# Kernel tuning notes

Hardware: AMD Instinct MI355X
Metric: run time of the kernel (lower is better)

The kernel has to match this reference:

```python
import jax, jax.numpy as jnp
import numpy as np

B, L, F, H, D, Z, NF = 256, 256, 38, 512, 512, 16, 20
LOG2PI = float(np.log(2.0 * np.pi))


def setup_inputs() -> dict:
    ks = jax.random.split(jax.random.key(0), 32)
    def p(i, shape, s=0.05):
        return jax.random.normal(ks[i], shape, jnp.float32) * s
    return {
        "x": jax.random.normal(ks[0], (B, L, F), jnp.float32),
        "phi_Wih": p(1, (3 * H, F)), "phi_Whh": p(2, (3 * H, H)),
        "phi_bih": p(3, (3 * H,)), "phi_bhh": p(4, (3 * H,)),
        "phi_W1": p(5, (D, H + Z)), "phi_b1": p(6, (D,)),
        "phi_W2": p(7, (D, D)), "phi_b2": p(8, (D,)),
        "zloc_W": p(9, (Z, D)), "zloc_b": p(10, (Z,)),
        "zscale_W": p(11, (Z, D)), "zscale_b": p(12, (Z,)),
        "pu": p(13, (NF, Z)), "pw": p(14, (NF, Z)), "pb": p(15, (NF,)),
        "th_Wih": p(16, (3 * H, Z)), "th_Whh": p(17, (3 * H, H)),
        "th_bih": p(18, (3 * H,)), "th_bhh": p(19, (3 * H,)),
        "th_W1": p(20, (D, H)), "th_b1": p(21, (D,)),
        "th_W2": p(22, (D, D)), "th_b2": p(23, (D,)),
        "xloc_W": p(24, (F, D)), "xloc_b": p(25, (F,)),
        "xscale_W": p(26, (F, D)), "xscale_b": p(27, (F,)),
    }


def _gru(x, h, Wih, Whh, bih, bhh):
    # torch.nn.GRUCell, gate order (r, z, n)
    gi = x @ Wih.T + bih
    gh = h @ Whh.T + bhh
    ir, iz, inn = jnp.split(gi, 3, axis=-1)
    hr, hz, hn = jnp.split(gh, 3, axis=-1)
    r = jax.nn.sigmoid(ir + hr)
    z = jax.nn.sigmoid(iz + hz)
    n = jnp.tanh(inn + r * hn)
    return (1.0 - z) * n + z * h


def _normal_lp(x, loc, scale):
    return -0.5 * ((x - loc) / scale) ** 2 - jnp.log(scale) - 0.5 * LOG2PI


def _forward(x, phi_Wih, phi_Whh, phi_bih, phi_bhh, phi_W1, phi_b1, phi_W2, phi_b2,
             zloc_W, zloc_b, zscale_W, zscale_b, pu, pw, pb,
             th_Wih, th_Whh, th_bih, th_bhh, th_W1, th_b1, th_W2, th_b2,
             xloc_W, xloc_b, xscale_W, xscale_b):
    b, l, f = x.shape
    z_dim = zloc_b.shape[0]
    h_dim = phi_bih.shape[0] // 3
    # fixed rsample noise (reference determinism): z posterior base sample + prior sample
    kz, kp = jax.random.split(jax.random.key(42))
    eps_z = jax.random.normal(kz, (l, b, z_dim), x.dtype)
    eps_p = jax.random.normal(kp, (l, b, z_dim), x.dtype)
    xs = jnp.swapaxes(x, 0, 1)  # [L, B, F]

    # Pyro Planar: u_hat = u + (softplus(w.u) - 1 - w.u) * w / ||w||^2
    wnorm2 = jnp.sum(pw * pw, axis=-1)                     # [NF]
    wu = jnp.sum(pw * pu, axis=-1)                         # [NF]
    uhat = pu + ((jax.nn.softplus(wu) - 1.0 - wu) / wnorm2)[:, None] * pw  # [NF, Z]
    uhat_w = jnp.sum(uhat * pw, axis=-1)                   # [NF]

    def flows(z0):
        def fstep(z, fp):
            w, uh, bb, uw = fp
            a = jnp.tanh(z @ w + bb)                       # [B]
            z_new = z + uh[None, :] * a[:, None]
            ld = jnp.log(jnp.abs(1.0 + (1.0 - a * a) * uw) + 1e-12)  # [B]
            return z_new, ld
        z_fin, lds = jax.lax.scan(fstep, z0, (pw, uhat, pb, uhat_w))
        return z_fin, jnp.sum(lds)

    def step(carry, inp):
        phi_h, th_h, zt, recon, kld = carry
        xt, ez, ep = inp
        phi_h = _gru(xt, phi_h, phi_Wih, phi_Whh, phi_bih, phi_bhh)
        h1 = jax.nn.relu(jnp.concatenate([phi_h, zt], axis=-1) @ phi_W1.T + phi_b1)
        h2 = h1 @ phi_W2.T + phi_b2
        z_loc = h2 @ zloc_W.T + zloc_b
        z_scale = jax.nn.softplus(h2 @ zscale_W.T + zscale_b) + 1e-6
        z0 = z_loc + z_scale * ez
        base_lp = jnp.sum(-0.5 * ez * ez - jnp.log(z_scale) - 0.5 * LOG2PI)
        zt_new, logdet = flows(z0)
        th_h = _gru(zt_new, th_h, th_Wih, th_Whh, th_bih, th_bhh)
        g1 = jax.nn.relu(th_h @ th_W1.T + th_b1)
        g2 = g1 @ th_W2.T + th_b2
        y_loc = g2 @ xloc_W.T + xloc_b
        y_scale = jax.nn.softplus(g2 @ xscale_W.T + xscale_b) + 1e-6
        recon = recon - jnp.sum(_normal_lp(xt, y_loc, y_scale))
        # prior log_prob of its own rsample depends only on eps (loc cancels)
        prior_lp = jnp.sum(-0.5 * ep * ep - 0.5 * LOG2PI)
        kld = kld + (base_lp - logdet) - prior_lp
        return (phi_h, th_h, zt_new, recon, kld), y_loc

    init = (jnp.zeros((b, h_dim), x.dtype), jnp.zeros((b, h_dim), x.dtype),
            jnp.zeros((b, z_dim), x.dtype), jnp.zeros((), x.dtype), jnp.zeros((), x.dtype))
    (_, _, _, recon, kld), y_loc = jax.lax.scan(step, init, (xs, eps_z, eps_p))
    return jnp.swapaxes(y_loc, 0, 1), recon, kld


def reference(x, phi_Wih, phi_Whh, phi_bih, phi_bhh, phi_W1, phi_b1, phi_W2, phi_b2,
              zloc_W, zloc_b, zscale_W, zscale_b, pu, pw, pb,
              th_Wih, th_Whh, th_bih, th_bhh, th_W1, th_b1, th_W2, th_b2,
              xloc_W, xloc_b, xscale_W, xscale_b):
    return _forward(x, phi_Wih, phi_Whh, phi_bih, phi_bhh, phi_W1, phi_b1, phi_W2, phi_b2,
                    zloc_W, zloc_b, zscale_W, zscale_b, pu, pw, pb,
                    th_Wih, th_Whh, th_bih, th_bhh, th_W1, th_b1, th_W2, th_b2,
                    xloc_W, xloc_b, xscale_W, xscale_b)
```

## Files before the change

### kernel.cpp

```cpp
#include <hip/hip_runtime.h>
#include <stdint.h>
#include <math.h>

namespace {

constexpr int B = 256, L = 256, F = 38, H = 512, D = 512, Z = 16, NF = 20;
constexpr float LOG2PI_F = 1.8378770664093453f;
constexpr int LBZ = L * B * Z;
constexpr int HALF = LBZ / 2;
constexpr int HB = H * B;
constexpr int DB = D * B;
constexpr int ZB = Z * B;
constexpr int LFB = L * F * B;
constexpr int TC = 32;


__device__ __forceinline__ float sigmoidf_(float x) {
  return 1.0f / (1.0f + expf(-x));
}
__device__ __forceinline__ float softplusf_(float x) {
  return fmaxf(x, 0.0f) + log1pf(expf(-fabsf(x)));
}

__device__ __forceinline__ void waveReduceAtomicAdd(float* dst, float v, int tid) {
  #pragma unroll
  for (int off = 32; off > 0; off >>= 1) v += __shfl_down(v, off, 64);
  if ((tid & 63) == 0) atomicAdd(dst, v);
}


__host__ __device__ inline uint32_t rotl32_(uint32_t x, int d) {
  return (x << d) | (x >> (32 - d));
}

__host__ __device__ inline void threefry2x32_(uint32_t k0, uint32_t k1,
                                              uint32_t x0, uint32_t x1,
                                              uint32_t& o0, uint32_t& o1) {
  const uint32_t ks2 = k0 ^ k1 ^ 0x1BD11BDAu;
  uint32_t v0 = x0 + k0;
  uint32_t v1 = x1 + k1;
#define TF_RND(r) { v0 += v1; v1 = rotl32_(v1, r); v1 ^= v0; }
  TF_RND(13) TF_RND(15) TF_RND(26) TF_RND(6)
  v0 += k1;  v1 += ks2 + 1u;
  TF_RND(17) TF_RND(29) TF_RND(16) TF_RND(24)
  v0 += ks2; v1 += k0 + 2u;
  TF_RND(13) TF_RND(15) TF_RND(26) TF_RND(6)
  v0 += k0;  v1 += k1 + 3u;
  TF_RND(17) TF_RND(29) TF_RND(16) TF_RND(24)
  v0 += k1;  v1 += ks2 + 4u;
  TF_RND(13) TF_RND(15) TF_RND(26) TF_RND(6)
  v0 += ks2; v1 += k0 + 5u;
#undef TF_RND
  o0 = v0; o1 = v1;
}

__device__ __forceinline__ float erfinv_f_(float x) {
  float w = -log1pf(-x * x);
  float p;
  if (w < 5.0f) {
    w -= 2.5f;
    p = 2.81022636e-08f;
    p = fmaf(p, w, 3.43273939e-07f);
    p = fmaf(p, w, -3.5233877e-06f);
    p = fmaf(p, w, -4.39150654e-06f);
    p = fmaf(p, w, 0.00021858087f);
    p = fmaf(p, w, -0.00125372503f);
    p = fmaf(p, w, -0.00417768164f);
    p = fmaf(p, w, 0.246640727f);
    p = fmaf(p, w, 1.50140941f);
  } else {
    w = sqrtf(w) - 3.0f;
    p = -0.000200214257f;
    p = fmaf(p, w, 0.000100950558f);
    p = fmaf(p, w, 0.00134934322f);
    p = fmaf(p, w, -0.00367342844f);
    p = fmaf(p, w, 0.00573950773f);
    p = fmaf(p, w, -0.0076224613f);
    p = fmaf(p, w, 0.00943887047f);
    p = fmaf(p, w, 1.00167406f);
    p = fmaf(p, w, 2.83297682f);
  }
  return p * x;
}

__device__ __forceinline__ float bits_to_normal_(uint32_t bits) {
  uint32_t m = (bits >> 9) | 0x3f800000u;
  float f = __uint_as_float(m) - 1.0f;
  float u = f * 2.0f + (-0.99999994f);
  u = fmaxf(-0.99999994f, u);
  return 1.41421356f * erfinv_f_(u);
}

__device__ __forceinline__ float flows_dev(float zv[Z], const float* __restrict__ pu,
                                           const float* __restrict__ pw,
                                           const float* __restrict__ pb) {
  float ld = 0.0f;
  for (int f = 0; f < NF; ++f) {
    const float* w = pw + f * Z;
    const float* u = pu + f * Z;
    float wn2 = 0.0f, wu = 0.0f;
    #pragma unroll
    for (int i = 0; i < Z; ++i) { wn2 = fmaf(w[i], w[i], wn2); wu = fmaf(w[i], u[i], wu); }
    float coef = (softplusf_(wu) - 1.0f - wu) / wn2;
    float a_in = pb[f];
    #pragma unroll
    for (int i = 0; i < Z; ++i) a_in = fmaf(zv[i], w[i], a_in);
    float a = tanhf(a_in);
    float uw = 0.0f;
    #pragma unroll
    for (int i = 0; i < Z; ++i) {
      float uh = fmaf(coef, w[i], u[i]);
      uw = fmaf(uh, w[i], uw);
      zv[i] = fmaf(uh, a, zv[i]);
    }
    ld += logf(fabsf(1.0f + (1.0f - a * a) * uw) + 1e-12f);
  }
  return ld;
}


__global__ __launch_bounds__(256) void k_transpose_x(const float* __restrict__ x,
                                                     float* __restrict__ xT) {
  int idx = blockIdx.x * blockDim.x + threadIdx.x;
  int f = idx % F;
  int t = (idx / F) % L;
  int b = idx / (F * L);
  xT[(t * F + f) * B + b] = x[idx];
}

__global__ __launch_bounds__(256) void k_noise(float* __restrict__ eps_z,
                                               float* __restrict__ kld_acc,
                                               uint32_t kz0, uint32_t kz1,
                                               uint32_t kp0, uint32_t kp1) {
  int i = blockIdx.x * blockDim.x + threadIdx.x;
  uint32_t a0, a1, b0, b1;
  threefry2x32_(kz0, kz1, (uint32_t)i, (uint32_t)(i + HALF), a0, a1);
  float ez0 = bits_to_normal_(a0);
  float ez1 = bits_to_normal_(a1);
  eps_z[i] = ez0;
  eps_z[i + HALF] = ez1;
  threefry2x32_(kp0, kp1, (uint32_t)i, (uint32_t)(i + HALF), b0, b1);
  float ep0 = bits_to_normal_(b0);
  float ep1 = bits_to_normal_(b1);
  float local = -0.5f * (ez0 * ez0 + ez1 * ez1) + 0.5f * (ep0 * ep0 + ep1 * ep1);
  waveReduceAtomicAdd(kld_acc, local, threadIdx.x);
}

__global__ void k_finalize(const float* __restrict__ acc, float* __restrict__ out) {
  out[(size_t)B * L * F] = acc[1];
  out[(size_t)B * L * F + 1] = acc[0];
}

__global__ __launch_bounds__(256) void k_compose(
    const float* __restrict__ A, const float* __restrict__ bA,
    const float* __restrict__ W2, const float* __restrict__ b2,
    float* __restrict__ Wc, float* __restrict__ bc) {
  const int r = blockIdx.x;
  const int k = threadIdx.x;
  float acc0 = 0.f, acc1 = 0.f;
  for (int j = 0; j < D; ++j) {
    float a = A[(size_t)r * D + j];
    acc0 = fmaf(a, W2[(size_t)j * D + k], acc0);
    acc1 = fmaf(a, W2[(size_t)j * D + k + 256], acc1);
  }
  Wc[(size_t)r * D + k] = acc0;
  Wc[(size_t)r * D + k + 256] = acc1;
  float accb = 0.f;
  for (int j = k; j < D; j += 256) accb += A[(size_t)r * D + j] * b2[j];
  __shared__ float s[256];
  s[k] = accb;
  __syncthreads();
  for (int off = 128; off > 0; off >>= 1) {
    if (k < off) s[k] += s[k + off];
    __syncthreads();
  }
  if (k == 0) bc[r] = s[0] + bA[r];
}


struct GruArgs {
  const float* xin;
  const float* hT;
  const float* Wih;
  const float* Whh;
  const float* bih;
  const float* bhh;
  float* hout;
  float* zT_out;
  const float* pu;
  const float* pw;
  const float* pb;
  float* kld_acc;
  int w0h;
};

template<bool THETA>
__device__ __forceinline__ void gru_dev(const GruArgs& A,
                                        float (&red)[4][4][8][64]) {
  const int tid = threadIdx.x;
  const int lane = tid & 63;
  const int wv = __builtin_amdgcn_readfirstlane(tid >> 6);
  const int j0 = blockIdx.x * 8;
  const int b0 = blockIdx.y * 64;
  const int b = b0 + lane;
  constexpr int K1 = THETA ? Z : F;

  float accR[8], accZ[8], accNX[8], accNH[8];
  #pragma unroll
  for (int r = 0; r < 8; ++r) { accR[r] = 0.f; accZ[r] = 0.f; accNX[r] = 0.f; accNH[r] = 0.f; }

  float zv[Z];
  float ld = 0.0f;

  if (wv == 0) {
    const float* wr = A.Wih + (size_t)(0 * H + j0) * K1;
    const float* wz = A.Wih + (size_t)(1 * H + j0) * K1;
    const float* wn = A.Wih + (size_t)(2 * H + j0) * K1;
    if (THETA) {
      #pragma unroll
      for (int i = 0; i < Z; ++i) zv[i] = A.xin[i * B + b];
      ld = flows_dev(zv, A.pu, A.pw, A.pb);
      #pragma unroll
      for (int k = 0; k < Z; k += 4) {
        #pragma unroll
        for (int r = 0; r < 8; ++r) {
          const float4 w0 = *(const float4*)(wr + r * K1 + k);
          const float4 w1 = *(const float4*)(wz + r * K1 + k);
          const float4 w2 = *(const float4*)(wn + r * K1 + k);
          accR[r]  = fmaf(w0.x, zv[k], fmaf(w0.y, zv[k+1], fmaf(w0.z, zv[k+2], fmaf(w0.w, zv[k+3], accR[r]))));
          accZ[r]  = fmaf(w1.x, zv[k], fmaf(w1.y, zv[k+1], fmaf(w1.z, zv[k+2], fmaf(w1.w, zv[k+3], accZ[r]))));
          accNX[r] = fmaf(w2.x, zv[k], fmaf(w2.y, zv[k+1], fmaf(w2.z, zv[k+2], fmaf(w2.w, zv[k+3], accNX[r]))));
        }
      }
    } else {
      for (int k = 0; k < K1; ++k) {
        float a = A.xin[k * B + b];
        #pragma unroll
        for (int r = 0; r < 8; ++r) {
          accR[r]  = fmaf(wr[r * K1 + k], a, accR[r]);
          accZ[r]  = fmaf(wz[r * K1 + k], a, accZ[r]);
          accNX[r] = fmaf(wn[r * K1 + k], a, accNX[r]);
        }
      }
    }
  }

  const int rest = (H - A.w0h) / 3;
  const int hlo = (wv == 0) ? 0 : A.w0h + (wv - 1) * rest;
  const int hhi = (wv == 0) ? A.w0h : hlo + rest;
  {
    const float* vr = A.Whh + (size_t)(0 * H + j0) * H;
    const float* vz = A.Whh + (size_t)(1 * H + j0) * H;
    const float* vn = A.Whh + (size_t)(2 * H + j0) * H;
    #pragma unroll 2
    for (int k = hlo; k < hhi; k += 4) {
      const float a0 = A.hT[(size_t)(k + 0) * B + b];
      const float a1 = A.hT[(size_t)(k + 1) * B + b];
      const float a2 = A.hT[(size_t)(k + 2) * B + b];
      const float a3 = A.hT[(size_t)(k + 3) * B + b];
      #pragma unroll
      for (int r = 0; r < 8; ++r) {
        const float4 w0 = *(const float4*)(vr + (size_t)r * H + k);
        const float4 w1 = *(const float4*)(vz + (size_t)r * H + k);
        const float4 w2 = *(const float4*)(vn + (size_t)r * H + k);
        accR[r]  = fmaf(w0.x, a0, fmaf(w0.y, a1, fmaf(w0.z, a2, fmaf(w0.w, a3, accR[r]))));
        accZ[r]  = fmaf(w1.x, a0, fmaf(w1.y, a1, fmaf(w1.z, a2, fmaf(w1.w, a3, accZ[r]))));
        accNH[r] = fmaf(w2.x, a0, fmaf(w2.y, a1, fmaf(w2.z, a2, fmaf(w2.w, a3, accNH[r]))));
      }
    }
  }

  #pragma unroll
  for (int r = 0; r < 8; ++r) {
    red[wv][0][r][lane] = accR[r];
    red[wv][1][r][lane] = accZ[r];
    red[wv][2][r][lane] = accNX[r];
    red[wv][3][r][lane] = accNH[r];
  }

  if (THETA) {
    if (wv == 0 && blockIdx.x == 0) {
      #pragma unroll
      for (int i = 0; i < Z; ++i) A.zT_out[i * B + b] = zv[i];
      waveReduceAtomicAdd(A.kld_acc, -ld, lane);
    }
  }

  __syncthreads();

  #pragma unroll
  for (int it = tid; it < 512; it += 256) {
    const int r = it >> 6, l = it & 63;
    float sR = 0.f, sZ = 0.f, sNX = 0.f, sNH = 0.f;
    #pragma unroll
    for (int w = 0; w < 4; ++w) {
      sR  += red[w][0][r][l];
      sZ  += red[w][1][r][l];
      sNX += red[w][2][r][l];
      sNH += red[w][3][r][l];
    }
    const int j = j0 + r;
    const int bb = b0 + l;
    const float rg = sigmoidf_(sR + A.bih[j] + A.bhh[j]);
    const float zg = sigmoidf_(sZ + A.bih[H + j] + A.bhh[H + j]);
    const float ng = tanhf(sNX + A.bih[2 * H + j] + rg * (sNH + A.bhh[2 * H + j]));
    const float hp = A.hT[(size_t)j * B + bb];
    A.hout[(size_t)j * B + bb] = (1.0f - zg) * ng + zg * hp;
  }
}

__global__ __launch_bounds__(256) void k_gru_dual(GruArgs phi, GruArgs th, int mode) {
  __shared__ float red[4][4][8][64];
  const bool isTheta = (mode == 1) || (mode == 2 && blockIdx.z == 1);
  if (isTheta) gru_dev<true>(th, red);
  else         gru_dev<false>(phi, red);
}

__global__ __launch_bounds__(256) void k_lin(
    const float* __restrict__ A1, int K1v, long sA1,
    const float* __restrict__ A2, int K2v,
    const float* __restrict__ W, const float* __restrict__ bias,
    float* __restrict__ outp, long sOut, int relu) {
  const int tid = threadIdx.x;
  const int lane = tid & 63;
  const int wv = __builtin_amdgcn_readfirstlane(tid >> 6);
  const int r0 = blockIdx.x * 8;
  const int b0 = blockIdx.y * 64;
  const int b = b0 + lane;
  const int Kv = K1v + K2v;
  const float* A1p = A1 + (size_t)blockIdx.z * sA1;
  float* outpp = outp + (size_t)blockIdx.z * sOut;
  const int klo = wv * (Kv >> 2);
  const int khi = klo + (Kv >> 2);

  float acc[8];
  #pragma unroll
  for (int r = 0; r < 8; ++r) acc[r] = 0.f;

  const float* wbase = W + (size_t)r0 * Kv;
  {
    const int hi = khi < K1v ? khi : K1v;
    #pragma unroll 4
    for (int k = klo; k < hi; k += 4) {
      const float a0 = A1p[(size_t)(k + 0) * B + b];
      const float a1 = A1p[(size_t)(k + 1) * B + b];
      const float a2 = A1p[(size_t)(k + 2) * B + b];
      const float a3 = A1p[(size_t)(k + 3) * B + b];
      #pragma unroll
      for (int r = 0; r < 8; ++r) {
        const float4 w4 = *(const float4*)(wbase + (size_t)r * Kv + k);
        acc[r] = fmaf(w4.x, a0, fmaf(w4.y, a1, fmaf(w4.z, a2, fmaf(w4.w, a3, acc[r]))));
      }
    }
  }
  if (K2v) {
    const int lo = klo > K1v ? klo : K1v;
    for (int k = lo; k < khi; k += 4) {
      const float a0 = A2[(size_t)(k - K1v + 0) * B + b];
      const float a1 = A2[(size_t)(k - K1v + 1) * B + b];
      const float a2 = A2[(size_t)(k - K1v + 2) * B + b];
      const float a3 = A2[(size_t)(k - K1v + 3) * B + b];
      #pragma unroll
      for (int r = 0; r < 8; ++r) {
        const float4 w4 = *(const float4*)(wbase + (size_t)r * Kv + k);
        acc[r] = fmaf(w4.x, a0, fmaf(w4.y, a1, fmaf(w4.z, a2, fmaf(w4.w, a3, acc[r]))));
      }
    }
  }

  __shared__ float red[4][8][64];
  #pragma unroll
  for (int r = 0; r < 8; ++r) red[wv][r][lane] = acc[r];
  __syncthreads();

  #pragma unroll
  for (int it = tid; it < 512; it += 256) {
    int r = it >> 6, l = it & 63;
    float s = red[0][r][l] + red[1][r][l] + red[2][r][l] + red[3][r][l] + bias[r0 + r];
    if (relu) s = fmaxf(s, 0.f);
    outpp[(size_t)(r0 + r) * B + b0 + l] = s;
  }
}

__global__ __launch_bounds__(256) void k_zhead(
    const float* __restrict__ h1T,
    const float* __restrict__ Wzl, const float* __restrict__ bzl,
    const float* __restrict__ Wzs, const float* __restrict__ bzs,
    const float* __restrict__ eps_t,
    float* __restrict__ z0T, float* __restrict__ kld_acc) {
  const int tid = threadIdx.x;
  const int lane = tid & 63;
  const int wv = __builtin_amdgcn_readfirstlane(tid >> 6);
  const int z0q = blockIdx.x * 4;
  const int b0 = blockIdx.y * 64;
  const int b = b0 + lane;
  const int klo = wv * (D >> 2), khi = klo + (D >> 2);

  const float* wp[8];
  #pragma unroll
  for (int i = 0; i < 8; ++i) {
    int zz = z0q + (i >> 1);
    wp[i] = ((i & 1) ? Wzs : Wzl) + (size_t)zz * D;
  }
  float acc[8];
  #pragma unroll
  for (int i = 0; i < 8; ++i) acc[i] = 0.f;
  #pragma unroll 4
  for (int k = klo; k < khi; k += 4) {
    const float a0 = h1T[(size_t)(k + 0) * B + b];
    const float a1 = h1T[(size_t)(k + 1) * B + b];
    const float a2 = h1T[(size_t)(k + 2) * B + b];
    const float a3 = h1T[(size_t)(k + 3) * B + b];
    #pragma unroll
    for (int i = 0; i < 8; ++i) {
      const float4 w4 = *(const float4*)(wp[i] + k);
      acc[i] = fmaf(w4.x, a0, fmaf(w4.y, a1, fmaf(w4.z, a2, fmaf(w4.w, a3, acc[i]))));
    }
  }

  __shared__ float red[4][8][64];
  #pragma unroll
  for (int i = 0; i < 8; ++i) red[wv][i][lane] = acc[i];
  __syncthreads();

  int zi = tid >> 6, l = tid & 63;
  int zz = z0q + zi;
  int bb = b0 + l;
  float sl = red[0][2 * zi][l] + red[1][2 * zi][l] + red[2][2 * zi][l] + red[3][2 * zi][l]
             + bzl[zz];
  float ss = red[0][2 * zi + 1][l] + red[1][2 * zi + 1][l] + red[2][2 * zi + 1][l]
             + red[3][2 * zi + 1][l] + bzs[zz];
  float scale = softplusf_(ss) + 1e-6f;
  float ez = eps_t[bb * Z + zz];
  z0T[zz * B + bb] = sl + scale * ez;
  waveReduceAtomicAdd(kld_acc, -logf(scale), tid);
}

__global__ __launch_bounds__(256) void k_yhead(
    const float* __restrict__ g1base, long sG1, int t_base,
    const float* __restrict__ Wyl, const float* __restrict__ byl,
    const float* __restrict__ Wys, const float* __restrict__ bys,
    const float* __restrict__ xT,
    float* __restrict__ out_yloc, float* __restrict__ recon_acc) {
  const int tid = threadIdx.x;
  const int lane = tid & 63;
  const int wv = __builtin_amdgcn_readfirstlane(tid >> 6);
  const int t = t_base + blockIdx.z;
  const float* g1T = g1base + (size_t)blockIdx.z * sG1;
  const int f0 = blockIdx.x * 4;
  const int b0 = blockIdx.y * 64;
  const int b = b0 + lane;
  const int klo = wv * (D >> 2), khi = klo + (D >> 2);

  const float* wp[8];
  #pragma unroll
  for (int i = 0; i < 8; ++i) {
    int ff = f0 + (i >> 1);
    int fc = ff < F ? ff : 0;
    wp[i] = ((i & 1) ? Wys : Wyl) + (size_t)fc * D;
  }
  float acc[8];
  #pragma unroll
  for (int i = 0; i < 8; ++i) acc[i] = 0.f;
  #pragma unroll 4
  for (int k = klo; k < khi; k += 4) {
    const float a0 = g1T[(size_t)(k + 0) * B + b];
    const float a1 = g1T[(size_t)(k + 1) * B + b];
    const float a2 = g1T[(size_t)(k + 2) * B + b];
    const float a3 = g1T[(size_t)(k + 3) * B + b];
    #pragma unroll
    for (int i = 0; i < 8; ++i) {
      const float4 w4 = *(const float4*)(wp[i] + k);
      acc[i] = fmaf(w4.x, a0, fmaf(w4.y, a1, fmaf(w4.z, a2, fmaf(w4.w, a3, acc[i]))));
    }
  }

  __shared__ float red[4][8][64];
  #pragma unroll
  for (int i = 0; i < 8; ++i) red[wv][i][lane] = acc[i];
  __syncthreads();

  int fi = tid >> 6, l = tid & 63;
  int ff = f0 + fi;
  int bb = b0 + l;
  float nl = 0.0f;
  if (ff < F) {
    float loc = red[0][2 * fi][l] + red[1][2 * fi][l] + red[2][2 * fi][l] + red[3][2 * fi][l]
                + byl[ff];
    float sp = red[0][2 * fi + 1][l] + red[1][2 * fi + 1][l] + red[2][2 * fi + 1][l]
               + red[3][2 * fi + 1][l] + bys[ff];
    float scale = softplusf_(sp) + 1e-6f;
    out_yloc[((size_t)bb * L + t) * F + ff] = loc;
    float xv = xT[((size_t)t * F + ff) * B + bb];
    float d = (xv - loc) / scale;
    nl = 0.5f * d * d + logf(scale) + 0.5f * LOG2PI_F;
  }
  waveReduceAtomicAdd(recon_acc, nl, tid);
}

}

extern "C" void kernel_launch(void* const* d_in, const int* in_sizes, int n_in,
                              void* d_out, int out_size, void* d_ws, size_t ws_size,
                              hipStream_t stream) {
  const float* x        = (const float*)d_in[0];
  const float* phi_Wih  = (const float*)d_in[1];
  const float* phi_Whh  = (const float*)d_in[2];
  const float* phi_bih  = (const float*)d_in[3];
  const float* phi_bhh  = (const float*)d_in[4];
  const float* phi_W1   = (const float*)d_in[5];
  const float* phi_b1   = (const float*)d_in[6];
  const float* phi_W2   = (const float*)d_in[7];
  const float* phi_b2   = (const float*)d_in[8];
  const float* zloc_W   = (const float*)d_in[9];
  const float* zloc_b   = (const float*)d_in[10];
  const float* zscale_W = (const float*)d_in[11];
  const float* zscale_b = (const float*)d_in[12];
  const float* pu       = (const float*)d_in[13];
  const float* pw       = (const float*)d_in[14];
  const float* pb       = (const float*)d_in[15];
  const float* th_Wih   = (const float*)d_in[16];
  const float* th_Whh   = (const float*)d_in[17];
  const float* th_bih   = (const float*)d_in[18];
  const float* th_bhh   = (const float*)d_in[19];
  const float* th_W1    = (const float*)d_in[20];
  const float* th_b1    = (const float*)d_in[21];
  const float* th_W2    = (const float*)d_in[22];
  const float* th_b2    = (const float*)d_in[23];
  const float* xloc_W   = (const float*)d_in[24];
  const float* xloc_b   = (const float*)d_in[25];
  const float* xscale_W = (const float*)d_in[26];
  const float* xscale_b = (const float*)d_in[27];

  float* out = (float*)d_out;
  float* ws = (float*)d_ws;

  float* acc   = ws;
  float* eps_z = ws + 64;
  float* xT    = eps_z + LBZ;
  float* hphi0 = xT + LFB;
  float* hphi1 = hphi0 + HB;
  float* zT    = hphi1 + HB;
  float* z0T   = zT + ZB;
  float* h1T   = z0T + ZB;
  float* g1T   = h1T + DB;
  float* Wzl   = g1T + DB;
  float* Wzs   = Wzl + Z * D;
  float* bzl   = Wzs + Z * D;
  float* bzs   = bzl + 64;
  float* Wyl   = bzs + 64;
  float* Wys   = Wyl + F * D;
  float* byl   = Wys + F * D;
  float* bys   = byl + 64;
  float* tailbase = bys + 64;

  size_t floatsA = (size_t)(tailbase - ws) + (size_t)(L + 1) * HB + (size_t)TC * DB;
  bool pathA = ws_size >= floatsA * sizeof(float);

  float* th_all = tailbase;
  float* g1_c   = th_all + (size_t)(L + 1) * HB;
  float* hth0   = tailbase;
  float* hth1   = tailbase + HB;

  hipMemsetAsync(acc, 0, 2 * sizeof(float), stream);
  hipMemsetAsync(hphi0, 0, (size_t)HB * sizeof(float), stream);
  hipMemsetAsync(zT, 0, (size_t)ZB * sizeof(float), stream);
  if (pathA) hipMemsetAsync(th_all, 0, (size_t)HB * sizeof(float), stream);
  else       hipMemsetAsync(hth1, 0, (size_t)HB * sizeof(float), stream);

  uint32_t a0, a1, b0, b1;
  threefry2x32_(0u, 42u, 0u, 2u, a0, a1);
  threefry2x32_(0u, 42u, 1u, 3u, b0, b1);
  const uint32_t kz0 = a0, kz1 = b0, kp0 = a1, kp1 = b1;

  k_transpose_x<<<(B * L * F) / 256, 256, 0, stream>>>(x, xT);
  k_noise<<<HALF / 256, 256, 0, stream>>>(eps_z, acc, kz0, kz1, kp0, kp1);

  k_compose<<<Z, 256, 0, stream>>>(zloc_W, zloc_b, phi_W2, phi_b2, Wzl, bzl);
  k_compose<<<Z, 256, 0, stream>>>(zscale_W, zscale_b, phi_W2, phi_b2, Wzs, bzs);
  k_compose<<<F, 256, 0, stream>>>(xloc_W, xloc_b, th_W2, th_b2, Wyl, byl);
  k_compose<<<F, 256, 0, stream>>>(xscale_W, xscale_b, th_W2, th_b2, Wys, bys);

  const dim3 gLin(D / 8, B / 64, 1);
  const dim3 gZ(Z / 4, B / 64, 1);

  for (int t = 0; t <= L; ++t) {
    const bool hasPhi = (t < L);
    const bool hasTh  = (t >= 1);

    GruArgs pa = {};
    GruArgs ta = {};
    float* phi_new = (t & 1) ? hphi0 : hphi1;
    if (hasPhi) {
      pa.xin  = xT + (size_t)t * F * B;
      pa.hT   = (t & 1) ? hphi1 : hphi0;
      pa.hout = phi_new;
      pa.Wih = phi_Wih; pa.Whh = phi_Whh; pa.bih = phi_bih; pa.bhh = phi_bhh;
      pa.w0h = 92;
    }
    float* th_new = nullptr;
    if (hasTh) {
      ta.xin  = z0T;
      ta.hT   = pathA ? th_all + (size_t)(t - 1) * HB
                      : ((t & 1) ? hth1 : hth0);
      th_new  = pathA ? th_all + (size_t)t * HB
                      : ((t & 1) ? hth0 : hth1);
      ta.hout = th_new;
      ta.Wih = th_Wih; ta.Whh = th_Whh; ta.bih = th_bih; ta.bhh = th_bhh;
      ta.zT_out = zT; ta.pu = pu; ta.pw = pw; ta.pb = pb; ta.kld_acc = acc;
      ta.w0h = 80;
    }

    const int mode = (hasPhi && hasTh) ? 2 : (hasTh ? 1 : 0);
    dim3 gG(H / 8, B / 64, mode == 2 ? 2 : 1);
    k_gru_dual<<<gG, 256, 0, stream>>>(pa, ta, mode);

    if (hasPhi) {
      k_lin<<<gLin, 256, 0, stream>>>(phi_new, H, 0, zT, Z, phi_W1, phi_b1, h1T, 0, 1);
      k_zhead<<<gZ, 256, 0, stream>>>(h1T, Wzl, bzl, Wzs, bzs,
                                      eps_z + (size_t)t * B * Z, z0T, acc);
    }

    if (!pathA && hasTh) {
      k_lin<<<gLin, 256, 0, stream>>>(th_new, H, 0, nullptr, 0, th_W1, th_b1, g1T, 0, 1);
      dim3 gy((F + 3) / 4, B / 64, 1);
      k_yhead<<<gy, 256, 0, stream>>>(g1T, 0, t - 1, Wyl, byl, Wys, bys,
                                      xT, out, acc + 1);
    }
  }

  if (pathA) {
    for (int c = 0; c < L / TC; ++c) {
      const float* thh = th_all + (size_t)(c * TC + 1) * HB;
      dim3 g1(D / 8, B / 64, TC);
      k_lin<<<g1, 256, 0, stream>>>(thh, H, HB, nullptr, 0, th_W1, th_b1, g1_c, DB, 1);
      dim3 gy((F + 3) / 4, B / 64, TC);
      k_yhead<<<gy, 256, 0, stream>>>(g1_c, DB, c * TC, Wyl, byl, Wys, bys,
                                      xT, out, acc + 1);
    }
  }

  k_finalize<<<1, 1, 0, stream>>>(acc, out);
}
```

Measured before the change: 23.90 ms.

## Replace per-timestep kernel launches with a persistent kernel using grid barriers

```diff
diff --git a/kernel.cpp b/kernel.cpp
--- a/kernel.cpp
+++ b/kernel.cpp
@@ -12,7 +12,7 @@
 constexpr int DB = D * B;
 constexpr int ZB = Z * B;
 constexpr int LFB = L * F * B;
-constexpr int TC = 32;
+constexpr int GRIDN = 512;
 
 
 __device__ __forceinline__ float sigmoidf_(float x) {
@@ -26,6 +26,25 @@
   #pragma unroll
   for (int off = 32; off > 0; off >>= 1) v += __shfl_down(v, off, 64);
   if ((tid & 63) == 0) atomicAdd(dst, v);
+}
+
+__device__ __forceinline__ void grid_sync_(uint32_t* bar) {
+  __syncthreads();
+  if (threadIdx.x == 0) {
+    __threadfence();
+    uint32_t g = __hip_atomic_load(&bar[1], __ATOMIC_RELAXED, __HIP_MEMORY_SCOPE_AGENT);
+    uint32_t a = __hip_atomic_fetch_add(&bar[0], 1u, __ATOMIC_RELAXED, __HIP_MEMORY_SCOPE_AGENT);
+    if (a == (uint32_t)(GRIDN - 1)) {
+      __hip_atomic_store(&bar[0], 0u, __ATOMIC_RELAXED, __HIP_MEMORY_SCOPE_AGENT);
+      __threadfence();
+      __hip_atomic_fetch_add(&bar[1], 1u, __ATOMIC_RELAXED, __HIP_MEMORY_SCOPE_AGENT);
+    } else {
+      while (__hip_atomic_load(&bar[1], __ATOMIC_RELAXED, __HIP_MEMORY_SCOPE_AGENT) == g)
+        __builtin_amdgcn_s_sleep(2);
+    }
+    __threadfence();
+  }
+  __syncthreads();
 }
 
 
@@ -177,31 +196,19 @@
   if (k == 0) bc[r] = s[0] + bA[r];
 }
 
-
-struct GruArgs {
-  const float* xin;
-  const float* hT;
-  const float* Wih;
-  const float* Whh;
-  const float* bih;
-  const float* bhh;
-  float* hout;
-  float* zT_out;
-  const float* pu;
-  const float* pw;
-  const float* pb;
-  float* kld_acc;
-  int w0h;
-};
-
 template<bool THETA>
-__device__ __forceinline__ void gru_dev(const GruArgs& A,
-                                        float (&red)[4][4][8][64]) {
+__device__ __forceinline__ void gru_phase(
+    int blk2, const float* __restrict__ xin, const float* __restrict__ hT,
+    const float* __restrict__ Wih, const float* __restrict__ Whh,
+    const float* __restrict__ bih, const float* __restrict__ bhh,
+    float* __restrict__ hout, float* zT_out,
+    const float* pu, const float* pw, const float* pb, float* kld_acc,
+    int w0h, float (&red)[4][4][8][64]) {
   const int tid = threadIdx.x;
   const int lane = tid & 63;
   const int wv = __builtin_amdgcn_readfirstlane(tid >> 6);
-  const int j0 = blockIdx.x * 8;
-  const int b0 = blockIdx.y * 64;
+  const int j0 = (blk2 >> 2) * 8;
+  const int b0 = (blk2 & 3) * 64;
   const int b = b0 + lane;
   constexpr int K1 = THETA ? Z : F;
 
@@ -213,13 +220,13 @@
   float ld = 0.0f;
 
   if (wv == 0) {
-    const float* wr = A.Wih + (size_t)(0 * H + j0) * K1;
-    const float* wz = A.Wih + (size_t)(1 * H + j0) * K1;
-    const float* wn = A.Wih + (size_t)(2 * H + j0) * K1;
+    const float* wr = Wih + (size_t)(0 * H + j0) * K1;
+    const float* wz = Wih + (size_t)(1 * H + j0) * K1;
+    const float* wn = Wih + (size_t)(2 * H + j0) * K1;
     if (THETA) {
       #pragma unroll
-      for (int i = 0; i < Z; ++i) zv[i] = A.xin[i * B + b];
-      ld = flows_dev(zv, A.pu, A.pw, A.pb);
+      for (int i = 0; i < Z; ++i) zv[i] = xin[i * B + b];
+      ld = flows_dev(zv, pu, pw, pb);
       #pragma unroll
       for (int k = 0; k < Z; k += 4) {
         #pragma unroll
@@ -234,7 +241,7 @@
       }
     } else {
       for (int k = 0; k < K1; ++k) {
-        float a = A.xin[k * B + b];
+        float a = xin[k * B + b];
         #pragma unroll
         for (int r = 0; r < 8; ++r) {
           accR[r]  = fmaf(wr[r * K1 + k], a, accR[r]);
@@ -245,19 +252,19 @@
     }
   }
 
-  const int rest = (H - A.w0h) / 3;
-  const int hlo = (wv == 0) ? 0 : A.w0h + (wv - 1) * rest;
-  const int hhi = (wv == 0) ? A.w0h : hlo + rest;
+  const int rest = (H - w0h) / 3;
+  const int hlo = (wv == 0) ? 0 : w0h + (wv - 1) * rest;
+  const int hhi = (wv == 0) ? w0h : hlo + rest;
   {
-    const float* vr = A.Whh + (size_t)(0 * H + j0) * H;
-    const float* vz = A.Whh + (size_t)(1 * H + j0) * H;
-    const float* vn = A.Whh + (size_t)(2 * H + j0) * H;
+    const float* vr = Whh + (size_t)(0 * H + j0) * H;
+    const float* vz = Whh + (size_t)(1 * H + j0) * H;
+    const float* vn = Whh + (size_t)(2 * H + j0) * H;
     #pragma unroll 2
     for (int k = hlo; k < hhi; k += 4) {
-      const float a0 = A.hT[(size_t)(k + 0) * B + b];
-      const float a1 = A.hT[(size_t)(k + 1) * B + b];
-      const float a2 = A.hT[(size_t)(k + 2) * B + b];
-      const float a3 = A.hT[(size_t)(k + 3) * B + b];
+      const float a0 = hT[(size_t)(k + 0) * B + b];
+      const float a1 = hT[(size_t)(k + 1) * B + b];
+      const float a2 = hT[(size_t)(k + 2) * B + b];
+      const float a3 = hT[(size_t)(k + 3) * B + b];
       #pragma unroll
       for (int r = 0; r < 8; ++r) {
         const float4 w0 = *(const float4*)(vr + (size_t)r * H + k);
@@ -279,10 +286,10 @@
   }
 
   if (THETA) {
-    if (wv == 0 && blockIdx.x == 0) {
+    if (wv == 0 && j0 == 0) {
       #pragma unroll
-      for (int i = 0; i < Z; ++i) A.zT_out[i * B + b] = zv[i];
-      waveReduceAtomicAdd(A.kld_acc, -ld, lane);
+      for (int i = 0; i < Z; ++i) zT_out[i * B + b] = zv[i];
+      waveReduceAtomicAdd(kld_acc, -ld, lane);
     }
   }
 
@@ -301,35 +308,26 @@
     }
     const int j = j0 + r;
     const int bb = b0 + l;
-    const float rg = sigmoidf_(sR + A.bih[j] + A.bhh[j]);
-    const float zg = sigmoidf_(sZ + A.bih[H + j] + A.bhh[H + j]);
-    const float ng = tanhf(sNX + A.bih[2 * H + j] + rg * (sNH + A.bhh[2 * H + j]));
-    const float hp = A.hT[(size_t)j * B + bb];
-    A.hout[(size_t)j * B + bb] = (1.0f - zg) * ng + zg * hp;
-  }
-}
-
-__global__ __launch_bounds__(256) void k_gru_dual(GruArgs phi, GruArgs th, int mode) {
-  __shared__ float red[4][4][8][64];
-  const bool isTheta = (mode == 1) || (mode == 2 && blockIdx.z == 1);
-  if (isTheta) gru_dev<true>(th, red);
-  else         gru_dev<false>(phi, red);
-}
-
-__global__ __launch_bounds__(256) void k_lin(
-    const float* __restrict__ A1, int K1v, long sA1,
+    const float rg = sigmoidf_(sR + bih[j] + bhh[j]);
+    const float zg = sigmoidf_(sZ + bih[H + j] + bhh[H + j]);
+    const float ng = tanhf(sNX + bih[2 * H + j] + rg * (sNH + bhh[2 * H + j]));
+    const float hp = hT[(size_t)j * B + bb];
+    hout[(size_t)j * B + bb] = (1.0f - zg) * ng + zg * hp;
+  }
+}
+
+__device__ __forceinline__ void lin8_phase(
+    int blk2, const float* __restrict__ A1, int K1v,
     const float* __restrict__ A2, int K2v,
     const float* __restrict__ W, const float* __restrict__ bias,
-    float* __restrict__ outp, long sOut, int relu) {
+    float* __restrict__ outp, int relu, float* shbase) {
   const int tid = threadIdx.x;
   const int lane = tid & 63;
   const int wv = __builtin_amdgcn_readfirstlane(tid >> 6);
-  const int r0 = blockIdx.x * 8;
-  const int b0 = blockIdx.y * 64;
+  const int r0 = (blk2 >> 2) * 8;
+  const int b0 = (blk2 & 3) * 64;
   const int b = b0 + lane;
   const int Kv = K1v + K2v;
-  const float* A1p = A1 + (size_t)blockIdx.z * sA1;
-  float* outpp = outp + (size_t)blockIdx.z * sOut;
   const int klo = wv * (Kv >> 2);
   const int khi = klo + (Kv >> 2);
 
@@ -342,10 +340,10 @@
     const int hi = khi < K1v ? khi : K1v;
     #pragma unroll 4
     for (int k = klo; k < hi; k += 4) {
-      const float a0 = A1p[(size_t)(k + 0) * B + b];
-      const float a1 = A1p[(size_t)(k + 1) * B + b];
-      const float a2 = A1p[(size_t)(k + 2) * B + b];
-      const float a3 = A1p[(size_t)(k + 3) * B + b];
+      const float a0 = A1[(size_t)(k + 0) * B + b];
+      const float a1 = A1[(size_t)(k + 1) * B + b];
+      const float a2 = A1[(size_t)(k + 2) * B + b];
+      const float a3 = A1[(size_t)(k + 3) * B + b];
       #pragma unroll
       for (int r = 0; r < 8; ++r) {
         const float4 w4 = *(const float4*)(wbase + (size_t)r * Kv + k);
@@ -368,31 +366,32 @@
     }
   }
 
-  __shared__ float red[4][8][64];
-  #pragma unroll
-  for (int r = 0; r < 8; ++r) red[wv][r][lane] = acc[r];
+  float* red = shbase;
+  #pragma unroll
+  for (int r = 0; r < 8; ++r) red[(wv * 8 + r) * 64 + lane] = acc[r];
   __syncthreads();
 
   #pragma unroll
   for (int it = tid; it < 512; it += 256) {
     int r = it >> 6, l = it & 63;
-    float s = red[0][r][l] + red[1][r][l] + red[2][r][l] + red[3][r][l] + bias[r0 + r];
+    float s = red[(0 * 8 + r) * 64 + l] + red[(1 * 8 + r) * 64 + l]
+            + red[(2 * 8 + r) * 64 + l] + red[(3 * 8 + r) * 64 + l] + bias[r0 + r];
     if (relu) s = fmaxf(s, 0.f);
-    outpp[(size_t)(r0 + r) * B + b0 + l] = s;
-  }
-}
-
-__global__ __launch_bounds__(256) void k_zhead(
-    const float* __restrict__ h1T,
+    outp[(size_t)(r0 + r) * B + b0 + l] = s;
+  }
+}
+
+__device__ __forceinline__ void zhead_phase(
+    int blk2, const float* __restrict__ h1T,
     const float* __restrict__ Wzl, const float* __restrict__ bzl,
     const float* __restrict__ Wzs, const float* __restrict__ bzs,
-    const float* __restrict__ eps_t,
-    float* __restrict__ z0T, float* __restrict__ kld_acc) {
+    const float* __restrict__ eps_t, float* __restrict__ z0T,
+    float* kld_acc, float* shbase) {
   const int tid = threadIdx.x;
   const int lane = tid & 63;
   const int wv = __builtin_amdgcn_readfirstlane(tid >> 6);
-  const int z0q = blockIdx.x * 4;
-  const int b0 = blockIdx.y * 64;
+  const int z0q = (blk2 >> 2) * 4;
+  const int b0 = (blk2 & 3) * 64;
   const int b = b0 + lane;
   const int klo = wv * (D >> 2), khi = klo + (D >> 2);
 
@@ -418,37 +417,35 @@
     }
   }
 
-  __shared__ float red[4][8][64];
-  #pragma unroll
-  for (int i = 0; i < 8; ++i) red[wv][i][lane] = acc[i];
+  float* red = shbase;
+  #pragma unroll
+  for (int i = 0; i < 8; ++i) red[(wv * 8 + i) * 64 + lane] = acc[i];
   __syncthreads();
 
   int zi = tid >> 6, l = tid & 63;
   int zz = z0q + zi;
   int bb = b0 + l;
-  float sl = red[0][2 * zi][l] + red[1][2 * zi][l] + red[2][2 * zi][l] + red[3][2 * zi][l]
-             + bzl[zz];
-  float ss = red[0][2 * zi + 1][l] + red[1][2 * zi + 1][l] + red[2][2 * zi + 1][l]
-             + red[3][2 * zi + 1][l] + bzs[zz];
+  float sl = red[(0 * 8 + 2 * zi) * 64 + l] + red[(1 * 8 + 2 * zi) * 64 + l]
+           + red[(2 * 8 + 2 * zi) * 64 + l] + red[(3 * 8 + 2 * zi) * 64 + l] + bzl[zz];
+  float ss = red[(0 * 8 + 2 * zi + 1) * 64 + l] + red[(1 * 8 + 2 * zi + 1) * 64 + l]
+           + red[(2 * 8 + 2 * zi + 1) * 64 + l] + red[(3 * 8 + 2 * zi + 1) * 64 + l] + bzs[zz];
   float scale = softplusf_(ss) + 1e-6f;
   float ez = eps_t[bb * Z + zz];
   z0T[zz * B + bb] = sl + scale * ez;
   waveReduceAtomicAdd(kld_acc, -logf(scale), tid);
 }
 
-__global__ __launch_bounds__(256) void k_yhead(
-    const float* __restrict__ g1base, long sG1, int t_base,
+__device__ __forceinline__ void yhead_phase(
+    int blk2, int t, const float* __restrict__ g1T,
     const float* __restrict__ Wyl, const float* __restrict__ byl,
     const float* __restrict__ Wys, const float* __restrict__ bys,
-    const float* __restrict__ xT,
-    float* __restrict__ out_yloc, float* __restrict__ recon_acc) {
+    const float* __restrict__ xT, float* __restrict__ out_yloc,
+    float* recon_acc, float* shbase) {
   const int tid = threadIdx.x;
   const int lane = tid & 63;
   const int wv = __builtin_amdgcn_readfirstlane(tid >> 6);
-  const int t = t_base + blockIdx.z;
-  const float* g1T = g1base + (size_t)blockIdx.z * sG1;
-  const int f0 = blockIdx.x * 4;
-  const int b0 = blockIdx.y * 64;
+  const int f0 = (blk2 >> 2) * 4;
+  const int b0 = (blk2 & 3) * 64;
   const int b = b0 + lane;
   const int klo = wv * (D >> 2), khi = klo + (D >> 2);
 
@@ -475,9 +472,9 @@
     }
   }
 
-  __shared__ float red[4][8][64];
-  #pragma unroll
-  for (int i = 0; i < 8; ++i) red[wv][i][lane] = acc[i];
+  float* red = shbase;
+  #pragma unroll
+  for (int i = 0; i < 8; ++i) red[(wv * 8 + i) * 64 + lane] = acc[i];
   __syncthreads();
 
   int fi = tid >> 6, l = tid & 63;
@@ -485,10 +482,10 @@
   int bb = b0 + l;
   float nl = 0.0f;
   if (ff < F) {
-    float loc = red[0][2 * fi][l] + red[1][2 * fi][l] + red[2][2 * fi][l] + red[3][2 * fi][l]
-                + byl[ff];
-    float sp = red[0][2 * fi + 1][l] + red[1][2 * fi + 1][l] + red[2][2 * fi + 1][l]
-               + red[3][2 * fi + 1][l] + bys[ff];
+    float loc = red[(0 * 8 + 2 * fi) * 64 + l] + red[(1 * 8 + 2 * fi) * 64 + l]
+              + red[(2 * 8 + 2 * fi) * 64 + l] + red[(3 * 8 + 2 * fi) * 64 + l] + byl[ff];
+    float sp = red[(0 * 8 + 2 * fi + 1) * 64 + l] + red[(1 * 8 + 2 * fi + 1) * 64 + l]
+             + red[(2 * 8 + 2 * fi + 1) * 64 + l] + red[(3 * 8 + 2 * fi + 1) * 64 + l] + bys[ff];
     float scale = softplusf_(sp) + 1e-6f;
     out_yloc[((size_t)bb * L + t) * F + ff] = loc;
     float xv = xT[((size_t)t * F + ff) * B + bb];
@@ -496,6 +493,64 @@
     nl = 0.5f * d * d + logf(scale) + 0.5f * LOG2PI_F;
   }
   waveReduceAtomicAdd(recon_acc, nl, tid);
+}
+
+struct PP {
+  const float *xT, *eps_z;
+  const float *phi_Wih, *phi_Whh, *phi_bih, *phi_bhh, *phi_W1, *phi_b1;
+  const float *th_Wih, *th_Whh, *th_bih, *th_bhh, *th_W1, *th_b1;
+  const float *Wzl, *bzl, *Wzs, *bzs, *Wyl, *byl, *Wys, *bys;
+  const float *pu, *pw, *pb;
+  float *hphi0, *hphi1, *hth0, *hth1, *zT, *z0T, *h1T, *g1T, *acc, *out;
+  uint32_t* bar;
+};
+
+__global__ __launch_bounds__(256, 2) void k_persist(PP P) {
+  __shared__ float red[4][4][8][64];
+  const int blk = blockIdx.x;
+  float* sh = &red[0][0][0][0];
+
+  for (int t = 0; t <= L; ++t) {
+    float* hphi_c = (t & 1) ? P.hphi1 : P.hphi0;
+    float* hphi_n = (t & 1) ? P.hphi0 : P.hphi1;
+    float* hth_c  = (t & 1) ? P.hth1 : P.hth0;
+    float* hth_n  = (t & 1) ? P.hth0 : P.hth1;
+
+    if (blk < 256) {
+      if (t < L)
+        gru_phase<false>(blk, P.xT + (size_t)t * F * B, hphi_c,
+                         P.phi_Wih, P.phi_Whh, P.phi_bih, P.phi_bhh,
+                         hphi_n, nullptr, nullptr, nullptr, nullptr, nullptr,
+                         92, red);
+    } else {
+      if (t >= 1)
+        gru_phase<true>(blk - 256, P.z0T, hth_c,
+                        P.th_Wih, P.th_Whh, P.th_bih, P.th_bhh,
+                        hth_n, P.zT, P.pu, P.pw, P.pb, P.acc,
+                        80, red);
+    }
+    grid_sync_(P.bar);
+
+    if (blk < 256) {
+      if (t < L)
+        lin8_phase(blk, hphi_n, H, P.zT, Z, P.phi_W1, P.phi_b1, P.h1T, 1, sh);
+    } else {
+      if (t >= 1)
+        lin8_phase(blk - 256, hth_n, H, nullptr, 0, P.th_W1, P.th_b1, P.g1T, 1, sh);
+    }
+    grid_sync_(P.bar);
+
+    if (blk < 16) {
+      if (t < L)
+        zhead_phase(blk, P.h1T, P.Wzl, P.bzl, P.Wzs, P.bzs,
+                    P.eps_z + (size_t)t * B * Z, P.z0T, P.acc, sh);
+    } else if (blk >= 64 && blk < 104) {
+      if (t >= 1)
+        yhead_phase(blk - 64, t - 1, P.g1T, P.Wyl, P.byl, P.Wys, P.bys,
+                    P.xT, P.out, P.acc + 1, sh);
+    }
+    if (t < L) grid_sync_(P.bar);
+  }
 }
 
 }
@@ -536,11 +591,14 @@
   float* ws = (float*)d_ws;
 
   float* acc   = ws;
+  uint32_t* bar = (uint32_t*)(ws + 32);
   float* eps_z = ws + 64;
   float* xT    = eps_z + LBZ;
   float* hphi0 = xT + LFB;
   float* hphi1 = hphi0 + HB;
-  float* zT    = hphi1 + HB;
+  float* hth0  = hphi1 + HB;
+  float* hth1  = hth0 + HB;
+  float* zT    = hth1 + HB;
   float* z0T   = zT + ZB;
   float* h1T   = z0T + ZB;
   float* g1T   = h1T + DB;
@@ -552,21 +610,11 @@
   float* Wys   = Wyl + F * D;
   float* byl   = Wys + F * D;
   float* bys   = byl + 64;
-  float* tailbase = bys + 64;
-
-  size_t floatsA = (size_t)(tailbase - ws) + (size_t)(L + 1) * HB + (size_t)TC * DB;
-  bool pathA = ws_size >= floatsA * sizeof(float);
-
-  float* th_all = tailbase;
-  float* g1_c   = th_all + (size_t)(L + 1) * HB;
-  float* hth0   = tailbase;
-  float* hth1   = tailbase + HB;
-
-  hipMemsetAsync(acc, 0, 2 * sizeof(float), stream);
+
+  hipMemsetAsync(acc, 0, 64 * sizeof(float), stream);
   hipMemsetAsync(hphi0, 0, (size_t)HB * sizeof(float), stream);
+  hipMemsetAsync(hth1, 0, (size_t)HB * sizeof(float), stream);
   hipMemsetAsync(zT, 0, (size_t)ZB * sizeof(float), stream);
-  if (pathA) hipMemsetAsync(th_all, 0, (size_t)HB * sizeof(float), stream);
-  else       hipMemsetAsync(hth1, 0, (size_t)HB * sizeof(float), stream);
 
   uint32_t a0, a1, b0, b1;
   threefry2x32_(0u, 42u, 0u, 2u, a0, a1);
@@ -581,64 +629,20 @@
   k_compose<<<F, 256, 0, stream>>>(xloc_W, xloc_b, th_W2, th_b2, Wyl, byl);
   k_compose<<<F, 256, 0, stream>>>(xscale_W, xscale_b, th_W2, th_b2, Wys, bys);
 
-  const dim3 gLin(D / 8, B / 64, 1);
-  const dim3 gZ(Z / 4, B / 64, 1);
-
-  for (int t = 0; t <= L; ++t) {
-    const bool hasPhi = (t < L);
-    const bool hasTh  = (t >= 1);
-
-    GruArgs pa = {};
-    GruArgs ta = {};
-    float* phi_new = (t & 1) ? hphi0 : hphi1;
-    if (hasPhi) {
-      pa.xin  = xT + (size_t)t * F * B;
-      pa.hT   = (t & 1) ? hphi1 : hphi0;
-      pa.hout = phi_new;
-      pa.Wih = phi_Wih; pa.Whh = phi_Whh; pa.bih = phi_bih; pa.bhh = phi_bhh;
-      pa.w0h = 92;
-    }
-    float* th_new = nullptr;
-    if (hasTh) {
-      ta.xin  = z0T;
-      ta.hT   = pathA ? th_all + (size_t)(t - 1) * HB
-                      : ((t & 1) ? hth1 : hth0);
-      th_new  = pathA ? th_all + (size_t)t * HB
-                      : ((t & 1) ? hth0 : hth1);
-      ta.hout = th_new;
-      ta.Wih = th_Wih; ta.Whh = th_Whh; ta.bih = th_bih; ta.bhh = th_bhh;
-      ta.zT_out = zT; ta.pu = pu; ta.pw = pw; ta.pb = pb; ta.kld_acc = acc;
-      ta.w0h = 80;
-    }
-
-    const int mode = (hasPhi && hasTh) ? 2 : (hasTh ? 1 : 0);
-    dim3 gG(H / 8, B / 64, mode == 2 ? 2 : 1);
-    k_gru_dual<<<gG, 256, 0, stream>>>(pa, ta, mode);
-
-    if (hasPhi) {
-      k_lin<<<gLin, 256, 0, stream>>>(phi_new, H, 0, zT, Z, phi_W1, phi_b1, h1T, 0, 1);
-      k_zhead<<<gZ, 256, 0, stream>>>(h1T, Wzl, bzl, Wzs, bzs,
-                                      eps_z + (size_t)t * B * Z, z0T, acc);
-    }
-
-    if (!pathA && hasTh) {
-      k_lin<<<gLin, 256, 0, stream>>>(th_new, H, 0, nullptr, 0, th_W1, th_b1, g1T, 0, 1);
-      dim3 gy((F + 3) / 4, B / 64, 1);
-      k_yhead<<<gy, 256, 0, stream>>>(g1T, 0, t - 1, Wyl, byl, Wys, bys,
-                                      xT, out, acc + 1);
-    }
-  }
-
-  if (pathA) {
-    for (int c = 0; c < L / TC; ++c) {
-      const float* thh = th_all + (size_t)(c * TC + 1) * HB;
-      dim3 g1(D / 8, B / 64, TC);
-      k_lin<<<g1, 256, 0, stream>>>(thh, H, HB, nullptr, 0, th_W1, th_b1, g1_c, DB, 1);
-      dim3 gy((F + 3) / 4, B / 64, TC);
-      k_yhead<<<gy, 256, 0, stream>>>(g1_c, DB, c * TC, Wyl, byl, Wys, bys,
-                                      xT, out, acc + 1);
-    }
-  }
+  PP P;
+  P.xT = xT; P.eps_z = eps_z;
+  P.phi_Wih = phi_Wih; P.phi_Whh = phi_Whh; P.phi_bih = phi_bih; P.phi_bhh = phi_bhh;
+  P.phi_W1 = phi_W1; P.phi_b1 = phi_b1;
+  P.th_Wih = th_Wih; P.th_Whh = th_Whh; P.th_bih = th_bih; P.th_bhh = th_bhh;
+  P.th_W1 = th_W1; P.th_b1 = th_b1;
+  P.Wzl = Wzl; P.bzl = bzl; P.Wzs = Wzs; P.bzs = bzs;
+  P.Wyl = Wyl; P.byl = byl; P.Wys = Wys; P.bys = bys;
+  P.pu = pu; P.pw = pw; P.pb = pb;
+  P.hphi0 = hphi0; P.hphi1 = hphi1; P.hth0 = hth0; P.hth1 = hth1;
+  P.zT = zT; P.z0T = z0T; P.h1T = h1T; P.g1T = g1T;
+  P.acc = acc; P.out = out; P.bar = bar;
+
+  k_persist<<<GRIDN, 256, 0, stream>>>(P);
 
   k_finalize<<<1, 1, 0, stream>>>(acc, out);
 }
```

New measurement: 73.50 ms. 3.08x slower.
